# Kernel optimization log

Measured on AMD Instinct MI355X. Metric: run time of the kernel, lower is better.

## Reference

```python
import jax, jax.numpy as jnp
import numpy as np

D = 1024   # input_size / width
H = 1024   # hidden_size / lru_width
TW = 4     # conv1d temporal width (Griffin default)
C_GATE = 8.0


def setup_inputs() -> dict:
    key = jax.random.key(0)
    ks = jax.random.split(key, 12)
    B, T = 8, 4096
    sd = 1.0 / np.sqrt(D)
    sh = 1.0 / np.sqrt(H)
    return {
        "input_bxtxd": jax.random.normal(ks[0], (B, T, D), jnp.float32),
        "w_x": jax.random.normal(ks[1], (D, H), jnp.float32) * sd,
        "b_x": jnp.zeros((H,), jnp.float32),
        "w_y": jax.random.normal(ks[2], (D, H), jnp.float32) * sd,
        "b_y": jnp.zeros((H,), jnp.float32),
        "conv_w": jax.random.normal(ks[3], (TW, H), jnp.float32) * 0.5,
        "conv_b": jnp.zeros((H,), jnp.float32),
        "gi_w": jax.random.normal(ks[4], (H, H), jnp.float32) * sh,
        "gi_b": jnp.zeros((H,), jnp.float32),
        "ga_w": jax.random.normal(ks[5], (H, H), jnp.float32) * sh,
        "ga_b": jnp.zeros((H,), jnp.float32),
        # a_param > 0 so a = exp(-c*gate*softplus(a_param)) lies in (0,1)
        "a_param": jax.random.uniform(ks[6], (H,), jnp.float32, 2.0, 6.0),
    }


def reference(input_bxtxd, w_x, b_x, w_y, b_y, conv_w, conv_b,
              gi_w, gi_b, ga_w, ga_b, a_param):
    x = input_bxtxd                      # [B,T,D], batch_first
    B, T, _ = x.shape

    # x branch: linear_x -> causal depthwise conv1d (zero cache) -> RG-LRU
    x1 = jnp.einsum("btd,dh->bth", x, w_x) + b_x            # [B,T,H]
    xp = jnp.pad(x1, ((0, 0), (TW - 1, 0), (0, 0)))          # causal pad
    x2 = sum(conv_w[i] * xp[:, i:i + T, :] for i in range(TW)) + conv_b

    # RG-LRU gates (num_heads=1 -> full linear)
    gate_x = jax.nn.sigmoid(jnp.einsum("bth,hk->btk", x2, gi_w) + gi_b)
    gate_a = jax.nn.sigmoid(jnp.einsum("bth,hk->btk", x2, ga_w) + ga_b)
    log_a = -C_GATE * gate_a * jax.nn.softplus(a_param)      # [B,T,H]
    a = jnp.exp(log_a)
    multiplier = jnp.sqrt(jnp.maximum(1.0 - jnp.exp(2.0 * log_a), 0.0))
    # segment_pos = arange(T): reset at t == 0
    multiplier = multiplier.at[:, 0, :].set(1.0)
    a = a.at[:, 0, :].set(0.0)
    normalized_x = gate_x * x2 * multiplier                  # [B,T,H]

    # linear recurrence h_t = a_t * h_{t-1} + normalized_x_t (h_{-1}=0)
    def combine(c1, c2):
        a1, h1 = c1
        a2, h2 = c2
        return a1 * a2, h2 + a2 * h1

    _, h = jax.lax.associative_scan(combine, (a, normalized_x), axis=1)

    # y branch and output gating
    y = jax.nn.gelu(jnp.einsum("btd,dh->bth", x, w_y) + b_y, approximate=False)
    out = h * y                                              # [B,T,H]
    hn = h[:, -1, :]                                         # last state
    return out, h, hn
```

## Files before the change

kernel.cpp:

```cpp
#include <hip/hip_runtime.h>
#include <math.h>


#define B_ 8
#define T_ 4096
#define H_ 1024
#define M_ (B_ * T_)
#define NC_ 128
#define CL_ 32

typedef _Float16 half8 __attribute__((ext_vector_type(8)));
typedef _Float16 half4 __attribute__((ext_vector_type(4)));
typedef float    f32x4 __attribute__((ext_vector_type(4)));

#define BAR() __builtin_amdgcn_s_barrier()
#define SCHED0 __builtin_amdgcn_sched_barrier(0)
#define VMW(N) do { asm volatile("s_waitcnt vmcnt(" #N ")"); SCHED0; } while (0)
#define MFMA16(a, b, c) __builtin_amdgcn_mfma_f32_16x16x32_f16((a), (b), (c), 0, 0, 0)

__device__ __forceinline__ void load16_lds(const _Float16* g, _Float16* l) {
  __builtin_amdgcn_global_load_lds(
      (const __attribute__((address_space(1))) void*)g,
      (__attribute__((address_space(3))) void*)l, 16, 0, 0);
}

__global__ __launch_bounds__(256) void transpose_cvt(
    const float* __restrict__ sA, const float* __restrict__ sB,
    _Float16* __restrict__ dst) {
  __shared__ float tile[32][33];
  int bn = blockIdx.x * 32;
  int bk = blockIdx.y * 32;
  const float* src = (bn < 1024) ? sA : sB;
  int nof = (bn < 1024) ? bn : bn - 1024;
  int c  = threadIdx.x & 31;
  int r0 = threadIdx.x >> 5;
#pragma unroll
  for (int i = 0; i < 4; ++i) {
    int r = r0 + i * 8;
    tile[r][c] = src[(size_t)(bk + r) * 1024 + nof + c];
  }
  __syncthreads();
#pragma unroll
  for (int i = 0; i < 4; ++i) {
    int nl = r0 + i * 8;
    dst[(size_t)(bn + nl) * 1024 + bk + c] = (_Float16)tile[c][nl];
  }
}

__global__ void prep_bias(const float* __restrict__ bx, const float* __restrict__ by,
                          const float* __restrict__ gib, const float* __restrict__ gab,
                          float* __restrict__ b1, float* __restrict__ b2) {
  int i = blockIdx.x * 1024 + threadIdx.x;
  if (i < 1024)      b1[i] = bx[i];
  else if (i < 2048) b1[i] = by[i - 1024];
  else if (i < 3072) b2[i - 2048] = gib[i - 2048];
  else               b2[i - 2048] = gab[i - 3072];
}

__global__ __launch_bounds__(256) void cvt_fp16(
    const float* __restrict__ x, _Float16* __restrict__ xh, long n4) {
  for (long i = (long)blockIdx.x * 256 + threadIdx.x; i < n4;
       i += (long)gridDim.x * 256) {
    f32x4 v = ((const f32x4*)x)[i];
    half4 h;
#pragma unroll
    for (int e = 0; e < 4; ++e) h[e] = (_Float16)v[e];
    ((half4*)xh)[i] = h;
  }
}

template <int MODE>
__global__ __launch_bounds__(512, 2) void gemm_kernel(
    const _Float16* __restrict__ A, const _Float16* __restrict__ Bt,
    const float* __restrict__ bias, const float* __restrict__ a_param,
    _Float16* __restrict__ C) {
  __shared__ _Float16 ldsA[32768];
  __shared__ _Float16 ldsB[32768];
  int tid  = threadIdx.x;
  int lane = tid & 63;
  int wave = tid >> 6;
  int l15 = lane & 15, g = lane >> 4;

  int nb = ((int)blockIdx.x & 7) * 128 + ((int)blockIdx.x >> 3);
  int m0 = (nb >> 3) * 256;
  int n0 = (nb & 7) * 256;
  int wm = wave >> 2;
  int wn = wave & 3;

  int gsrc = (tid & 3) ^ ((tid >> 3) & 3);
  const _Float16* pA = A  + (size_t)(m0 + (tid >> 2)) * 1024 + gsrc * 8;
  const _Float16* pB = Bt + (size_t)(n0 + (tid >> 2)) * 1024 + gsrc * 8;
  _Float16* stA = ldsA + wave * 512;
  _Float16* stB = ldsB + wave * 512;

#define STAGE_A(kt, kh)                                                       \
  do {                                                                        \
    const _Float16* s_ = pA + (kt) * 64 + (kh) * 32;                          \
    _Float16* d_ = stA + (((kt) & 1) * 2 + (kh)) * 8192;                      \
    load16_lds(s_, d_);                                    \
    load16_lds(s_ + 131072, d_ + 4096);                    \
  } while (0)
#define STAGE_B(kt, kh)                                                       \
  do {                                                                        \
    const _Float16* s_ = pB + (kt) * 64 + (kh) * 32;                          \
    _Float16* d_ = stB + (((kt) & 1) * 2 + (kh)) * 8192;                      \
    load16_lds(s_, d_);                                                       \
    load16_lds(s_ + 131072, d_ + 4096);                                       \
  } while (0)

  int jj8  = ((g ^ ((l15 >> 1) & 3)) << 3);
  int aoff = wm * 4096 + l15 * 32 + jj8;
  int boff = wn * 2048 + l15 * 32 + jj8;

  f32x4 acc[8][4];
#pragma unroll
  for (int i = 0; i < 8; ++i)
#pragma unroll
    for (int j = 0; j < 4; ++j) acc[i][j] = (f32x4){0.f, 0.f, 0.f, 0.f};

  half8 a0[4], a1[4], b[4];

#define KTILE(SL, ST0, ST1, ST2, ST3, W1, W2)                                 \
  do {                                                                        \
    const int pl = (SL) * 16384;                                              \
                                               \
    _Pragma("unroll") for (int q = 0; q < 4; ++q)                             \
      a0[q] = *(const half8*)(ldsA + pl + q * 512 + aoff);                    \
    _Pragma("unroll") for (int q = 0; q < 4; ++q)                             \
      b[q]  = *(const half8*)(ldsB + pl + q * 512 + boff);                    \
    ST0;                                                                      \
    BAR();                                                                    \
    __builtin_amdgcn_s_setprio(1);                                            \
    _Pragma("unroll") for (int q = 0; q < 4; ++q) {                           \
      acc[q][0] = MFMA16(a0[q], b[0], acc[q][0]);                             \
      acc[q][1] = MFMA16(a0[q], b[1], acc[q][1]);                             \
      acc[q][2] = MFMA16(a0[q], b[2], acc[q][2]);                             \
      acc[q][3] = MFMA16(a0[q], b[3], acc[q][3]);                             \
    }                                                                         \
    __builtin_amdgcn_s_setprio(0);                                            \
    BAR();                                                                    \
                                               \
    _Pragma("unroll") for (int q = 0; q < 4; ++q)                             \
      a1[q] = *(const half8*)(ldsA + pl + 2048 + q * 512 + aoff);             \
    ST1;                                                                      \
    BAR();                                                                    \
    __builtin_amdgcn_s_setprio(1);                                            \
    _Pragma("unroll") for (int q = 0; q < 4; ++q) {                           \
      acc[4 + q][0] = MFMA16(a1[q], b[0], acc[4 + q][0]);                     \
      acc[4 + q][1] = MFMA16(a1[q], b[1], acc[4 + q][1]);                     \
      acc[4 + q][2] = MFMA16(a1[q], b[2], acc[4 + q][2]);                     \
      acc[4 + q][3] = MFMA16(a1[q], b[3], acc[4 + q][3]);                     \
    }                                                                         \
    __builtin_amdgcn_s_setprio(0);                                            \
    W1;                                                                       \
    BAR();                                                                    \
                                               \
    _Pragma("unroll") for (int q = 0; q < 4; ++q)                             \
      a0[q] = *(const half8*)(ldsA + pl + 8192 + q * 512 + aoff);             \
    _Pragma("unroll") for (int q = 0; q < 4; ++q)                             \
      b[q]  = *(const half8*)(ldsB + pl + 8192 + q * 512 + boff);             \
    ST2;                                                                      \
    BAR();                                                                    \
    __builtin_amdgcn_s_setprio(1);                                            \
    _Pragma("unroll") for (int q = 0; q < 4; ++q) {                           \
      acc[q][0] = MFMA16(a0[q], b[0], acc[q][0]);                             \
      acc[q][1] = MFMA16(a0[q], b[1], acc[q][1]);                             \
      acc[q][2] = MFMA16(a0[q], b[2], acc[q][2]);                             \
      acc[q][3] = MFMA16(a0[q], b[3], acc[q][3]);                             \
    }                                                                         \
    __builtin_amdgcn_s_setprio(0);                                            \
    BAR();                                                                    \
                                               \
    _Pragma("unroll") for (int q = 0; q < 4; ++q)                             \
      a1[q] = *(const half8*)(ldsA + pl + 8192 + 2048 + q * 512 + aoff);      \
    ST3;                                                                      \
    BAR();                                                                    \
    __builtin_amdgcn_s_setprio(1);                                            \
    _Pragma("unroll") for (int q = 0; q < 4; ++q) {                           \
      acc[4 + q][0] = MFMA16(a1[q], b[0], acc[4 + q][0]);                     \
      acc[4 + q][1] = MFMA16(a1[q], b[1], acc[4 + q][1]);                     \
      acc[4 + q][2] = MFMA16(a1[q], b[2], acc[4 + q][2]);                     \
      acc[4 + q][3] = MFMA16(a1[q], b[3], acc[4 + q][3]);                     \
    }                                                                         \
    __builtin_amdgcn_s_setprio(0);                                            \
    W2;                                                                       \
    BAR();                                                                    \
  } while (0)

  STAGE_B(0, 0); STAGE_A(0, 0); STAGE_B(0, 1); STAGE_A(0, 1);
  STAGE_B(1, 0); STAGE_A(1, 0); STAGE_B(1, 1);
  VMW(10);
  BAR();

  for (int t = 0; t < 14; ++t) {
    KTILE((t & 1),
          STAGE_A(t + 1, 1), STAGE_B(t + 2, 0),
          STAGE_A(t + 2, 0), STAGE_B(t + 2, 1),
          VMW(10), VMW(10));
  }
  KTILE(0, STAGE_A(15, 1), (void)0, (void)0, (void)0, VMW(8), VMW(4));
  KTILE(1, (void)0, (void)0, (void)0, (void)0, VMW(0), (void)0);

  int   gn[4];
  float bs[4], sp[4];
#pragma unroll
  for (int nj = 0; nj < 4; ++nj) {
    gn[nj] = n0 + wn * 64 + nj * 16 + l15;
    bs[nj] = bias[gn[nj]];
    sp[nj] = 0.f;
    if (MODE == 1 && gn[nj] >= 1024)
      sp[nj] = log1pf(expf(a_param[gn[nj] - 1024]));
  }
#pragma unroll
  for (int mi = 0; mi < 8; ++mi) {
#pragma unroll
    for (int p = 0; p < 4; ++p) {
      int gm = m0 + wm * 128 + mi * 16 + g * 4 + p;
      size_t rowb = (size_t)gm * 2048;
#pragma unroll
      for (int nj = 0; nj < 4; ++nj) {
        float v = acc[mi][nj][p] + bs[nj];
        if (MODE == 1) {
          float s = 1.f / (1.f + expf(-v));
          if (gn[nj] < 1024) {
            v = s;
          } else {
            float av = expf(-8.f * s * sp[nj]);
            if ((gm & (T_ - 1)) == 0) av = 0.f;
            v = av;
          }
        }
        C[rowb + gn[nj]] = (_Float16)v;
      }
    }
  }
#undef STAGE_A
#undef STAGE_B
#undef KTILE
}

__global__ __launch_bounds__(256) void conv_kernel(
    const _Float16* __restrict__ g1, const float* __restrict__ cw,
    const float* __restrict__ cb, _Float16* __restrict__ x2) {
  int idx = blockIdx.x * 256 + threadIdx.x;
  int m  = idx >> 7;
  int hb = (idx & 127) * 8;
  int t  = m & (T_ - 1);
  float acc[8];
#pragma unroll
  for (int e = 0; e < 8; ++e) acc[e] = cb[hb + e];
#pragma unroll
  for (int j = 0; j < 4; ++j) {
    if (t >= j) {
      half8 xv = *(const half8*)&g1[(size_t)(m - j) * 2048 + hb];
      const float* w = &cw[(3 - j) * 1024 + hb];
#pragma unroll
      for (int e = 0; e < 8; ++e) acc[e] += w[e] * (float)xv[e];
    }
  }
  half8 o;
#pragma unroll
  for (int e = 0; e < 8; ++e) o[e] = (_Float16)acc[e];
  *(half8*)&x2[(size_t)m * 1024 + hb] = o;
}

__global__ __launch_bounds__(128) void scan1_kernel(
    const _Float16* __restrict__ g2, const _Float16* __restrict__ x2,
    float* __restrict__ cA, float* __restrict__ cH) {
  int bid = blockIdx.x;
  int b = bid >> 7, c = bid & 127;
  int h0 = threadIdx.x * 8;
  float A[8], Hh[8];
#pragma unroll
  for (int e = 0; e < 8; ++e) { A[e] = 1.f; Hh[e] = 0.f; }
  size_t mbase = (size_t)b * T_ + (size_t)c * CL_;
  for (int i = 0; i < CL_; ++i) {
    size_t m = mbase + i;
    half8 gx = *(const half8*)&g2[m * 2048 + h0];
    half8 av = *(const half8*)&g2[m * 2048 + 1024 + h0];
    half8 xv = *(const half8*)&x2[m * 1024 + h0];
#pragma unroll
    for (int e = 0; e < 8; ++e) {
      float a = (float)av[e];
      float mult = sqrtf(fmaxf(1.f - a * a, 0.f));
      float nx = (float)gx[e] * (float)xv[e] * mult;
      A[e] *= a;
      Hh[e] = nx + a * Hh[e];
    }
  }
  size_t o = (size_t)bid * 1024 + h0;
#pragma unroll
  for (int e = 0; e < 8; ++e) { cA[o + e] = A[e]; cH[o + e] = Hh[e]; }
}

__global__ void scanmid_kernel(const float* __restrict__ cA,
                               const float* __restrict__ cH,
                               float* __restrict__ carry) {
  int gidx = blockIdx.x * 256 + threadIdx.x;
  int b = gidx >> 10, h = gidx & 1023;
  float run = 0.f;
  for (int c = 0; c < NC_; ++c) {
    size_t o = ((size_t)(b * NC_ + c)) * 1024 + h;
    carry[o] = run;
    run = cH[o] + cA[o] * run;
  }
}

__global__ __launch_bounds__(128) void scan2_kernel(
    const _Float16* __restrict__ g2, const _Float16* __restrict__ x2,
    const _Float16* __restrict__ g1, const float* __restrict__ carry,
    float* __restrict__ outO, float* __restrict__ outH,
    float* __restrict__ outHn) {
  int bid = blockIdx.x;
  int b = bid >> 7, c = bid & 127;
  int h0 = threadIdx.x * 8;
  float Hh[8];
  {
    size_t o = (size_t)bid * 1024 + h0;
#pragma unroll
    for (int e = 0; e < 8; ++e) Hh[e] = carry[o + e];
  }
  size_t mbase = (size_t)b * T_ + (size_t)c * CL_;
  for (int i = 0; i < CL_; ++i) {
    size_t m = mbase + i;
    half8 gx = *(const half8*)&g2[m * 2048 + h0];
    half8 av = *(const half8*)&g2[m * 2048 + 1024 + h0];
    half8 xv = *(const half8*)&x2[m * 1024 + h0];
    half8 uv = *(const half8*)&g1[m * 2048 + 1024 + h0];
    f32x4 hO[2], oO[2];
#pragma unroll
    for (int e = 0; e < 8; ++e) {
      float a = (float)av[e];
      float mult = sqrtf(fmaxf(1.f - a * a, 0.f));
      float nx = (float)gx[e] * (float)xv[e] * mult;
      float v = nx + a * Hh[e];
      Hh[e] = v;
      float u = (float)uv[e];
      float y = 0.5f * u * (1.f + erff(u * 0.70710678118654752f));
      hO[e >> 2][e & 3] = v;
      oO[e >> 2][e & 3] = v * y;
    }
    size_t ob = m * 1024 + h0;
    *(f32x4*)&outH[ob]     = hO[0];
    *(f32x4*)&outH[ob + 4] = hO[1];
    *(f32x4*)&outO[ob]     = oO[0];
    *(f32x4*)&outO[ob + 4] = oO[1];
  }
  if (c == NC_ - 1) {
    size_t o = (size_t)b * 1024 + h0;
#pragma unroll
    for (int e = 0; e < 8; ++e) outHn[o + e] = Hh[e];
  }
}

extern "C" void kernel_launch(void* const* d_in, const int* in_sizes, int n_in,
                              void* d_out, int out_size, void* d_ws,
                              size_t ws_size, hipStream_t stream) {
  const float* x   = (const float*)d_in[0];
  const float* wx  = (const float*)d_in[1];
  const float* bx  = (const float*)d_in[2];
  const float* wy  = (const float*)d_in[3];
  const float* by  = (const float*)d_in[4];
  const float* cw  = (const float*)d_in[5];
  const float* cb  = (const float*)d_in[6];
  const float* giw = (const float*)d_in[7];
  const float* gib = (const float*)d_in[8];
  const float* gaw = (const float*)d_in[9];
  const float* gab = (const float*)d_in[10];
  const float* ap  = (const float*)d_in[11];

  char* ws = (char*)d_ws;
  size_t off = 0;
  auto alloc = [&](size_t bytes) {
    char* p = ws + off;
    off += (bytes + 255) & ~(size_t)255;
    return p;
  };
  _Float16* wT1 = (_Float16*)alloc((size_t)2048 * 1024 * 2);
  _Float16* wT2 = (_Float16*)alloc((size_t)2048 * 1024 * 2);
  float*    b1  = (float*)alloc(2048 * 4);
  float*    b2  = (float*)alloc(2048 * 4);
  _Float16* xh  = (_Float16*)alloc((size_t)M_ * 1024 * 2);
  _Float16* g2e = (_Float16*)alloc((size_t)M_ * 1024 * 2);
  (void)g2e;
  _Float16* g1o = (_Float16*)alloc((size_t)M_ * 2048 * 2);
  _Float16* x2h = (_Float16*)alloc((size_t)M_ * 1024 * 2);
  float* cA  = (float*)alloc((size_t)B_ * NC_ * 1024 * 4);
  float* cH  = (float*)alloc((size_t)B_ * NC_ * 1024 * 4);
  float* cin = (float*)alloc((size_t)B_ * NC_ * 1024 * 4);
  _Float16* g2o = xh;

  float* oO  = (float*)d_out;
  float* oH  = oO + (size_t)M_ * 1024;
  float* oHn = oO + (size_t)2 * M_ * 1024;

  transpose_cvt<<<dim3(64, 32), 256, 0, stream>>>(wx, wy, wT1);
  transpose_cvt<<<dim3(64, 32), 256, 0, stream>>>(giw, gaw, wT2);
  prep_bias<<<4, 1024, 0, stream>>>(bx, by, gib, gab, b1, b2);
  cvt_fp16<<<2048, 256, 0, stream>>>(x, xh, (long)M_ * 1024 / 4);

  gemm_kernel<0><<<1024, 512, 0, stream>>>(xh, wT1, b1, nullptr, g1o);
  conv_kernel<<<16384, 256, 0, stream>>>(g1o, cw, cb, x2h);
  gemm_kernel<1><<<1024, 512, 0, stream>>>(x2h, wT2, b2, ap, g2o);

  scan1_kernel<<<B_ * NC_, 128, 0, stream>>>(g2o, x2h, cA, cH);
  scanmid_kernel<<<32, 256, 0, stream>>>(cA, cH, cin);
  scan2_kernel<<<B_ * NC_, 128, 0, stream>>>(g2o, x2h, g1o, cin, oO, oH, oHn);
}
```

Baseline: 627.3 us.

## Restructure 256-tile GEMM pipeline barriers and use simple 128-tile GEMM for gates

The 256x256 GEMM's staging schedule is reworked: A and B halves are staged together, and the per-subtile barriers are merged into two combined vmcnt/lgkmcnt wait-plus-barrier points per k-tile. The bias and softplus loads are hoisted before the main loop. The second (gate) GEMM is switched to a new, simpler 128x128-tile kernel with 4096 blocks and a single-buffered LDS loop. That kernel has no double buffering, so its global-to-LDS load latency is exposed, in exchange for more blocks and lower LDS use. Fewer barriers in the big GEMM also rely on the remaining waits being enough to avoid LDS hazards.

```diff
diff --git a/kernel.cpp b/kernel.cpp
--- a/kernel.cpp
+++ b/kernel.cpp
@@ -13,9 +13,14 @@
 typedef _Float16 half4 __attribute__((ext_vector_type(4)));
 typedef float    f32x4 __attribute__((ext_vector_type(4)));
 
-#define BAR() __builtin_amdgcn_s_barrier()
 #define SCHED0 __builtin_amdgcn_sched_barrier(0)
-#define VMW(N) do { asm volatile("s_waitcnt vmcnt(" #N ")"); SCHED0; } while (0)
+#define WAITBAR(N)                                                            \
+  do {                                                                        \
+    asm volatile("s_waitcnt vmcnt(" #N ") lgkmcnt(0)");                       \
+    SCHED0;                                                                   \
+    __builtin_amdgcn_s_barrier();                                             \
+    SCHED0;                                                                   \
+  } while (0)
 #define MFMA16(a, b, c) __builtin_amdgcn_mfma_f32_16x16x32_f16((a), (b), (c), 0, 0, 0)
 
 __device__ __forceinline__ void load16_lds(const _Float16* g, _Float16* l) {
@@ -70,7 +75,7 @@
 }
 
 template <int MODE>
-__global__ __launch_bounds__(512, 2) void gemm_kernel(
+__global__ __launch_bounds__(512, 2) void gemm256_kernel(
     const _Float16* __restrict__ A, const _Float16* __restrict__ Bt,
     const float* __restrict__ bias, const float* __restrict__ a_param,
     _Float16* __restrict__ C) {
@@ -86,6 +91,18 @@
   int n0 = (nb & 7) * 256;
   int wm = wave >> 2;
   int wn = wave & 3;
+
+  int   gn[4];
+  float bs[4], sp[4];
+#pragma unroll
+  for (int nj = 0; nj < 4; ++nj) {
+    gn[nj] = n0 + wn * 64 + nj * 16 + l15;
+    bs[nj] = bias[gn[nj]];
+    sp[nj] = 0.f;
+    if (MODE == 1 && gn[nj] >= 1024)
+      sp[nj] = log1pf(expf(a_param[gn[nj] - 1024]));
+  }
+  SCHED0;
 
   int gsrc = (tid & 3) ^ ((tid >> 3) & 3);
   const _Float16* pA = A  + (size_t)(m0 + (tid >> 2)) * 1024 + gsrc * 8;
@@ -120,16 +137,15 @@
 
   half8 a0[4], a1[4], b[4];
 
-#define KTILE(SL, ST0, ST1, ST2, ST3, W1, W2)                                 \
+#define KTILE(SL, ST0, ST2, WB1, WB2)                                         \
   do {                                                                        \
     const int pl = (SL) * 16384;                                              \
-                                               \
+                             \
     _Pragma("unroll") for (int q = 0; q < 4; ++q)                             \
       a0[q] = *(const half8*)(ldsA + pl + q * 512 + aoff);                    \
     _Pragma("unroll") for (int q = 0; q < 4; ++q)                             \
       b[q]  = *(const half8*)(ldsB + pl + q * 512 + boff);                    \
     ST0;                                                                      \
-    BAR();                                                                    \
     __builtin_amdgcn_s_setprio(1);                                            \
     _Pragma("unroll") for (int q = 0; q < 4; ++q) {                           \
       acc[q][0] = MFMA16(a0[q], b[0], acc[q][0]);                             \
@@ -138,12 +154,9 @@
       acc[q][3] = MFMA16(a0[q], b[3], acc[q][3]);                             \
     }                                                                         \
     __builtin_amdgcn_s_setprio(0);                                            \
-    BAR();                                                                    \
                                                \
     _Pragma("unroll") for (int q = 0; q < 4; ++q)                             \
       a1[q] = *(const half8*)(ldsA + pl + 2048 + q * 512 + aoff);             \
-    ST1;                                                                      \
-    BAR();                                                                    \
     __builtin_amdgcn_s_setprio(1);                                            \
     _Pragma("unroll") for (int q = 0; q < 4; ++q) {                           \
       acc[4 + q][0] = MFMA16(a1[q], b[0], acc[4 + q][0]);                     \
@@ -152,15 +165,13 @@
       acc[4 + q][3] = MFMA16(a1[q], b[3], acc[4 + q][3]);                     \
     }                                                                         \
     __builtin_amdgcn_s_setprio(0);                                            \
-    W1;                                                                       \
-    BAR();                                                                    \
-                                               \
+    WB1;                                                                      \
+                             \
     _Pragma("unroll") for (int q = 0; q < 4; ++q)                             \
       a0[q] = *(const half8*)(ldsA + pl + 8192 + q * 512 + aoff);             \
     _Pragma("unroll") for (int q = 0; q < 4; ++q)                             \
       b[q]  = *(const half8*)(ldsB + pl + 8192 + q * 512 + boff);             \
     ST2;                                                                      \
-    BAR();                                                                    \
     __builtin_amdgcn_s_setprio(1);                                            \
     _Pragma("unroll") for (int q = 0; q < 4; ++q) {                           \
       acc[q][0] = MFMA16(a0[q], b[0], acc[q][0]);                             \
@@ -169,12 +180,9 @@
       acc[q][3] = MFMA16(a0[q], b[3], acc[q][3]);                             \
     }                                                                         \
     __builtin_amdgcn_s_setprio(0);                                            \
-    BAR();                                                                    \
                                                \
     _Pragma("unroll") for (int q = 0; q < 4; ++q)                             \
       a1[q] = *(const half8*)(ldsA + pl + 8192 + 2048 + q * 512 + aoff);      \
-    ST3;                                                                      \
-    BAR();                                                                    \
     __builtin_amdgcn_s_setprio(1);                                            \
     _Pragma("unroll") for (int q = 0; q < 4; ++q) {                           \
       acc[4 + q][0] = MFMA16(a1[q], b[0], acc[4 + q][0]);                     \
@@ -183,34 +191,23 @@
       acc[4 + q][3] = MFMA16(a1[q], b[3], acc[4 + q][3]);                     \
     }                                                                         \
     __builtin_amdgcn_s_setprio(0);                                            \
-    W2;                                                                       \
-    BAR();                                                                    \
+    WB2;                                                                      \
   } while (0)
 
-  STAGE_B(0, 0); STAGE_A(0, 0); STAGE_B(0, 1); STAGE_A(0, 1);
-  STAGE_B(1, 0); STAGE_A(1, 0); STAGE_B(1, 1);
-  VMW(10);
-  BAR();
+  STAGE_A(0, 0); STAGE_B(0, 0);
+  STAGE_A(0, 1); STAGE_B(0, 1);
+  STAGE_A(1, 0); STAGE_B(1, 0);
+  WAITBAR(8);
 
   for (int t = 0; t < 14; ++t) {
     KTILE((t & 1),
-          STAGE_A(t + 1, 1), STAGE_B(t + 2, 0),
-          STAGE_A(t + 2, 0), STAGE_B(t + 2, 1),
-          VMW(10), VMW(10));
-  }
-  KTILE(0, STAGE_A(15, 1), (void)0, (void)0, (void)0, VMW(8), VMW(4));
-  KTILE(1, (void)0, (void)0, (void)0, (void)0, VMW(0), (void)0);
-
-  int   gn[4];
-  float bs[4], sp[4];
-#pragma unroll
-  for (int nj = 0; nj < 4; ++nj) {
-    gn[nj] = n0 + wn * 64 + nj * 16 + l15;
-    bs[nj] = bias[gn[nj]];
-    sp[nj] = 0.f;
-    if (MODE == 1 && gn[nj] >= 1024)
-      sp[nj] = log1pf(expf(a_param[gn[nj] - 1024]));
-  }
+          { STAGE_A(t + 1, 1); STAGE_B(t + 1, 1); },
+          { STAGE_A(t + 2, 0); STAGE_B(t + 2, 0); },
+          WAITBAR(8), WAITBAR(8));
+  }
+  KTILE(0, { STAGE_A(15, 1); STAGE_B(15, 1); }, (void)0, WAITBAR(8), WAITBAR(4));
+  KTILE(1, (void)0, (void)0, WAITBAR(0), (void)0);
+
 #pragma unroll
   for (int mi = 0; mi < 8; ++mi) {
 #pragma unroll
@@ -237,6 +234,104 @@
 #undef STAGE_A
 #undef STAGE_B
 #undef KTILE
+}
+
+template <int MODE>
+__global__ __launch_bounds__(256, 2) void gemm128_kernel(
+    const _Float16* __restrict__ A, const _Float16* __restrict__ Bt,
+    const float* __restrict__ bias, const float* __restrict__ a_param,
+    _Float16* __restrict__ C) {
+  __shared__ _Float16 sA[128 * 32];
+  __shared__ _Float16 sB[128 * 32];
+  const int K = 1024;
+  int tid  = threadIdx.x;
+  int lane = tid & 63;
+  int wave = tid >> 6;
+
+  int nb  = (int)blockIdx.x;
+  int per = (int)gridDim.x >> 3;
+  nb = (nb & 7) * per + (nb >> 3);
+  int mtile = nb >> 4;
+  int ntile = nb & 15;
+  int m0 = mtile * 128, n0 = ntile * 128;
+  int wm = wave >> 1, wn = wave & 1;
+
+  int row0 = tid >> 2, kg0 = tid & 3;
+  const _Float16* gA0 = A  + (size_t)(m0 + row0) * K + kg0 * 8;
+  const _Float16* gA1 = gA0 + (size_t)64 * K;
+  const _Float16* gB0 = Bt + (size_t)(n0 + row0) * K + kg0 * 8;
+  const _Float16* gB1 = gB0 + (size_t)64 * K;
+  _Float16* lA0 = sA + wave * 512;
+  _Float16* lA1 = sA + 2048 + wave * 512;
+  _Float16* lB0 = sB + wave * 512;
+  _Float16* lB1 = sB + 2048 + wave * 512;
+
+  f32x4 acc[4][4];
+#pragma unroll
+  for (int i = 0; i < 4; ++i)
+#pragma unroll
+    for (int j = 0; j < 4; ++j) acc[i][j] = (f32x4){0.f, 0.f, 0.f, 0.f};
+
+  const half8* sA8 = (const half8*)sA;
+  const half8* sB8 = (const half8*)sB;
+  int fa = (wm * 64 + (lane & 15)) * 4 + (lane >> 4);
+  int fb = (wn * 64 + (lane & 15)) * 4 + (lane >> 4);
+
+  for (int kk = 0; kk < 32; ++kk) {
+    int ko = kk * 32;
+    load16_lds(gA0 + ko, lA0);
+    load16_lds(gA1 + ko, lA1);
+    load16_lds(gB0 + ko, lB0);
+    load16_lds(gB1 + ko, lB1);
+    __syncthreads();
+    half8 af[4], bf[4];
+#pragma unroll
+    for (int mi = 0; mi < 4; ++mi) af[mi] = sA8[fa + mi * 64];
+#pragma unroll
+    for (int ni = 0; ni < 4; ++ni) bf[ni] = sB8[fb + ni * 64];
+#pragma unroll
+    for (int mi = 0; mi < 4; ++mi)
+#pragma unroll
+      for (int ni = 0; ni < 4; ++ni)
+        acc[mi][ni] = MFMA16(af[mi], bf[ni], acc[mi][ni]);
+    __syncthreads();
+  }
+
+  int lr = lane >> 4;
+  int lc = lane & 15;
+  int   gn[4];
+  float bs[4], sp[4];
+#pragma unroll
+  for (int ni = 0; ni < 4; ++ni) {
+    gn[ni] = n0 + wn * 64 + ni * 16 + lc;
+    bs[ni] = bias[gn[ni]];
+    sp[ni] = 0.f;
+    if (MODE == 1 && gn[ni] >= 1024)
+      sp[ni] = log1pf(expf(a_param[gn[ni] - 1024]));
+  }
+#pragma unroll
+  for (int mi = 0; mi < 4; ++mi) {
+#pragma unroll
+    for (int p = 0; p < 4; ++p) {
+      int gm = m0 + wm * 64 + mi * 16 + lr * 4 + p;
+      size_t rowb = (size_t)gm * 2048;
+#pragma unroll
+      for (int ni = 0; ni < 4; ++ni) {
+        float v = acc[mi][ni][p] + bs[ni];
+        if (MODE == 1) {
+          float s = 1.f / (1.f + expf(-v));
+          if (gn[ni] < 1024) {
+            v = s;
+          } else {
+            float av = expf(-8.f * s * sp[ni]);
+            if ((gm & (T_ - 1)) == 0) av = 0.f;
+            v = av;
+          }
+        }
+        C[rowb + gn[ni]] = (_Float16)v;
+      }
+    }
+  }
 }
 
 __global__ __launch_bounds__(256) void conv_kernel(
@@ -399,9 +494,9 @@
   prep_bias<<<4, 1024, 0, stream>>>(bx, by, gib, gab, b1, b2);
   cvt_fp16<<<2048, 256, 0, stream>>>(x, xh, (long)M_ * 1024 / 4);
 
-  gemm_kernel<0><<<1024, 512, 0, stream>>>(xh, wT1, b1, nullptr, g1o);
+  gemm256_kernel<0><<<1024, 512, 0, stream>>>(xh, wT1, b1, nullptr, g1o);
   conv_kernel<<<16384, 256, 0, stream>>>(g1o, cw, cb, x2h);
-  gemm_kernel<1><<<1024, 512, 0, stream>>>(x2h, wT2, b2, ap, g2o);
+  gemm128_kernel<1><<<4096, 256, 0, stream>>>(x2h, wT2, b2, ap, g2o);
 
   scan1_kernel<<<B_ * NC_, 128, 0, stream>>>(g2o, x2h, cA, cH);
   scanmid_kernel<<<32, 256, 0, stream>>>(cA, cH, cin);
```

Result: no change. 622.4 us (-0.8%).

## Cut GEMM barriers to two per k-tile and batch scan carry loads

Applied to the files above, without the earlier changes.

The GEMM main loop drops from eight barriers per k-tile to two combined waitcnt+barrier points. A and B stages are now issued together at two points per tile, and the bias/softplus epilogue loads are hoisted before the loop. The scanmid kernel loads eight chunk values at a time so the serial carry chain does not stall on each global load. Fewer barriers reduce sync stalls but risk LDS read/write hazards if the staging slots overlap with reads still in flight.

```diff
diff --git a/kernel.cpp b/kernel.cpp
--- a/kernel.cpp
+++ b/kernel.cpp
@@ -13,9 +13,14 @@
 typedef _Float16 half4 __attribute__((ext_vector_type(4)));
 typedef float    f32x4 __attribute__((ext_vector_type(4)));
 
-#define BAR() __builtin_amdgcn_s_barrier()
 #define SCHED0 __builtin_amdgcn_sched_barrier(0)
-#define VMW(N) do { asm volatile("s_waitcnt vmcnt(" #N ")"); SCHED0; } while (0)
+#define WAITBAR(N)                                                            \
+  do {                                                                        \
+    asm volatile("s_waitcnt vmcnt(" #N ") lgkmcnt(0)");                       \
+    SCHED0;                                                                   \
+    __builtin_amdgcn_s_barrier();                                             \
+    SCHED0;                                                                   \
+  } while (0)
 #define MFMA16(a, b, c) __builtin_amdgcn_mfma_f32_16x16x32_f16((a), (b), (c), 0, 0, 0)
 
 __device__ __forceinline__ void load16_lds(const _Float16* g, _Float16* l) {
@@ -70,7 +75,7 @@
 }
 
 template <int MODE>
-__global__ __launch_bounds__(512, 2) void gemm_kernel(
+__global__ __launch_bounds__(512, 2) void gemm256_kernel(
     const _Float16* __restrict__ A, const _Float16* __restrict__ Bt,
     const float* __restrict__ bias, const float* __restrict__ a_param,
     _Float16* __restrict__ C) {
@@ -86,6 +91,18 @@
   int n0 = (nb & 7) * 256;
   int wm = wave >> 2;
   int wn = wave & 3;
+
+  int   gn[4];
+  float bs[4], sp[4];
+#pragma unroll
+  for (int nj = 0; nj < 4; ++nj) {
+    gn[nj] = n0 + wn * 64 + nj * 16 + l15;
+    bs[nj] = bias[gn[nj]];
+    sp[nj] = 0.f;
+    if (MODE == 1 && gn[nj] >= 1024)
+      sp[nj] = log1pf(expf(a_param[gn[nj] - 1024]));
+  }
+  SCHED0;
 
   int gsrc = (tid & 3) ^ ((tid >> 3) & 3);
   const _Float16* pA = A  + (size_t)(m0 + (tid >> 2)) * 1024 + gsrc * 8;
@@ -120,16 +137,15 @@
 
   half8 a0[4], a1[4], b[4];
 
-#define KTILE(SL, ST0, ST1, ST2, ST3, W1, W2)                                 \
+#define KTILE(SL, ST0, ST2, WB1, WB2)                                         \
   do {                                                                        \
     const int pl = (SL) * 16384;                                              \
-                                               \
+                             \
     _Pragma("unroll") for (int q = 0; q < 4; ++q)                             \
       a0[q] = *(const half8*)(ldsA + pl + q * 512 + aoff);                    \
     _Pragma("unroll") for (int q = 0; q < 4; ++q)                             \
       b[q]  = *(const half8*)(ldsB + pl + q * 512 + boff);                    \
     ST0;                                                                      \
-    BAR();                                                                    \
     __builtin_amdgcn_s_setprio(1);                                            \
     _Pragma("unroll") for (int q = 0; q < 4; ++q) {                           \
       acc[q][0] = MFMA16(a0[q], b[0], acc[q][0]);                             \
@@ -138,12 +154,9 @@
       acc[q][3] = MFMA16(a0[q], b[3], acc[q][3]);                             \
     }                                                                         \
     __builtin_amdgcn_s_setprio(0);                                            \
-    BAR();                                                                    \
                                                \
     _Pragma("unroll") for (int q = 0; q < 4; ++q)                             \
       a1[q] = *(const half8*)(ldsA + pl + 2048 + q * 512 + aoff);             \
-    ST1;                                                                      \
-    BAR();                                                                    \
     __builtin_amdgcn_s_setprio(1);                                            \
     _Pragma("unroll") for (int q = 0; q < 4; ++q) {                           \
       acc[4 + q][0] = MFMA16(a1[q], b[0], acc[4 + q][0]);                     \
@@ -152,15 +165,13 @@
       acc[4 + q][3] = MFMA16(a1[q], b[3], acc[4 + q][3]);                     \
     }                                                                         \
     __builtin_amdgcn_s_setprio(0);                                            \
-    W1;                                                                       \
-    BAR();                                                                    \
-                                               \
+    WB1;                                                                      \
+                             \
     _Pragma("unroll") for (int q = 0; q < 4; ++q)                             \
       a0[q] = *(const half8*)(ldsA + pl + 8192 + q * 512 + aoff);             \
     _Pragma("unroll") for (int q = 0; q < 4; ++q)                             \
       b[q]  = *(const half8*)(ldsB + pl + 8192 + q * 512 + boff);             \
     ST2;                                                                      \
-    BAR();                                                                    \
     __builtin_amdgcn_s_setprio(1);                                            \
     _Pragma("unroll") for (int q = 0; q < 4; ++q) {                           \
       acc[q][0] = MFMA16(a0[q], b[0], acc[q][0]);                             \
@@ -169,12 +180,9 @@
       acc[q][3] = MFMA16(a0[q], b[3], acc[q][3]);                             \
     }                                                                         \
     __builtin_amdgcn_s_setprio(0);                                            \
-    BAR();                                                                    \
                                                \
     _Pragma("unroll") for (int q = 0; q < 4; ++q)                             \
       a1[q] = *(const half8*)(ldsA + pl + 8192 + 2048 + q * 512 + aoff);      \
-    ST3;                                                                      \
-    BAR();                                                                    \
     __builtin_amdgcn_s_setprio(1);                                            \
     _Pragma("unroll") for (int q = 0; q < 4; ++q) {                           \
       acc[4 + q][0] = MFMA16(a1[q], b[0], acc[4 + q][0]);                     \
@@ -183,34 +191,23 @@
       acc[4 + q][3] = MFMA16(a1[q], b[3], acc[4 + q][3]);                     \
     }                                                                         \
     __builtin_amdgcn_s_setprio(0);                                            \
-    W2;                                                                       \
-    BAR();                                                                    \
+    WB2;                                                                      \
   } while (0)
 
-  STAGE_B(0, 0); STAGE_A(0, 0); STAGE_B(0, 1); STAGE_A(0, 1);
-  STAGE_B(1, 0); STAGE_A(1, 0); STAGE_B(1, 1);
-  VMW(10);
-  BAR();
+  STAGE_A(0, 0); STAGE_B(0, 0);
+  STAGE_A(0, 1); STAGE_B(0, 1);
+  STAGE_A(1, 0); STAGE_B(1, 0);
+  WAITBAR(8);
 
   for (int t = 0; t < 14; ++t) {
     KTILE((t & 1),
-          STAGE_A(t + 1, 1), STAGE_B(t + 2, 0),
-          STAGE_A(t + 2, 0), STAGE_B(t + 2, 1),
-          VMW(10), VMW(10));
-  }
-  KTILE(0, STAGE_A(15, 1), (void)0, (void)0, (void)0, VMW(8), VMW(4));
-  KTILE(1, (void)0, (void)0, (void)0, (void)0, VMW(0), (void)0);
-
-  int   gn[4];
-  float bs[4], sp[4];
-#pragma unroll
-  for (int nj = 0; nj < 4; ++nj) {
-    gn[nj] = n0 + wn * 64 + nj * 16 + l15;
-    bs[nj] = bias[gn[nj]];
-    sp[nj] = 0.f;
-    if (MODE == 1 && gn[nj] >= 1024)
-      sp[nj] = log1pf(expf(a_param[gn[nj] - 1024]));
-  }
+          { STAGE_A(t + 1, 1); STAGE_B(t + 1, 1); },
+          { STAGE_A(t + 2, 0); STAGE_B(t + 2, 0); },
+          WAITBAR(8), WAITBAR(8));
+  }
+  KTILE(0, { STAGE_A(15, 1); STAGE_B(15, 1); }, (void)0, WAITBAR(8), WAITBAR(4));
+  KTILE(1, (void)0, (void)0, WAITBAR(0), (void)0);
+
 #pragma unroll
   for (int mi = 0; mi < 8; ++mi) {
 #pragma unroll
@@ -298,11 +295,22 @@
                                float* __restrict__ carry) {
   int gidx = blockIdx.x * 256 + threadIdx.x;
   int b = gidx >> 10, h = gidx & 1023;
+  const float* pa = cA + (size_t)b * NC_ * 1024 + h;
+  const float* ph = cH + (size_t)b * NC_ * 1024 + h;
+  float* pc = carry + (size_t)b * NC_ * 1024 + h;
   float run = 0.f;
-  for (int c = 0; c < NC_; ++c) {
-    size_t o = ((size_t)(b * NC_ + c)) * 1024 + h;
-    carry[o] = run;
-    run = cH[o] + cA[o] * run;
+  for (int c0 = 0; c0 < NC_; c0 += 8) {
+    float av[8], hv[8];
+#pragma unroll
+    for (int k = 0; k < 8; ++k) {
+      av[k] = pa[(size_t)(c0 + k) * 1024];
+      hv[k] = ph[(size_t)(c0 + k) * 1024];
+    }
+#pragma unroll
+    for (int k = 0; k < 8; ++k) {
+      pc[(size_t)(c0 + k) * 1024] = run;
+      run = hv[k] + av[k] * run;
+    }
   }
 }
 
@@ -399,9 +407,9 @@
   prep_bias<<<4, 1024, 0, stream>>>(bx, by, gib, gab, b1, b2);
   cvt_fp16<<<2048, 256, 0, stream>>>(x, xh, (long)M_ * 1024 / 4);
 
-  gemm_kernel<0><<<1024, 512, 0, stream>>>(xh, wT1, b1, nullptr, g1o);
+  gemm256_kernel<0><<<1024, 512, 0, stream>>>(xh, wT1, b1, nullptr, g1o);
   conv_kernel<<<16384, 256, 0, stream>>>(g1o, cw, cb, x2h);
-  gemm_kernel<1><<<1024, 512, 0, stream>>>(x2h, wT2, b2, ap, g2o);
+  gemm256_kernel<1><<<1024, 512, 0, stream>>>(x2h, wT2, b2, ap, g2o);
 
   scan1_kernel<<<B_ * NC_, 128, 0, stream>>>(g2o, x2h, cA, cH);
   scanmid_kernel<<<32, 256, 0, stream>>>(cA, cH, cin);
```

Result: no change. 615.2 us, median of 3 (-1.9%).
